# Performance work log

Measured on AMD Instinct MI355X. Metric: run time of the kernel, lower is better.

Reference implementation:

```python
import jax, jax.numpy as jnp
import numpy as np

N, E, D_X, D_H, K = 50000, 1600000, 128, 64, 4
NEG_SLOPE = 0.01  # torch nn.LeakyReLU() default


def setup_inputs() -> dict:
    key = jax.random.key(0)
    ks = jax.random.split(key, 8)
    x = jax.random.normal(ks[0], (N, D_X), dtype=jnp.float32)
    edge_index = jax.random.randint(ks[1], (2, E), 0, N, dtype=jnp.int64)
    s = 0.05
    Ww = jax.random.normal(ks[2], (K, D_H, D_X), dtype=jnp.float32) * s
    Wb = jax.random.normal(ks[3], (K, D_H), dtype=jnp.float32) * s
    aw = jax.random.normal(ks[4], (K, 1, 2 * D_H), dtype=jnp.float32) * s
    ab = jax.random.normal(ks[5], (K, 1), dtype=jnp.float32) * s
    Wo_w = jax.random.normal(ks[6], (D_H, K * D_H), dtype=jnp.float32) * s
    Wo_b = jax.random.normal(ks[7], (D_H,), dtype=jnp.float32) * s
    return {"edge_index": edge_index, "x": x, "Ww": Ww, "Wb": Wb,
            "aw": aw, "ab": ab, "Wo_w": Wo_w, "Wo_b": Wo_b}


def _single_head(x, src, dst, Ww_k, Wb_k, aw_k, ab_k):
    # Wx: [N, d_h] -- project once, gather per edge
    Wx = x @ Ww_k.T + Wb_k
    a_i = aw_k[0, :D_H]   # multiplies W(x_i) (target/dst)
    a_j = aw_k[0, D_H:]   # multiplies W(x_j) (source/src)
    si = Wx @ a_i         # [N]
    sj = Wx @ a_j         # [N]
    e = si[dst] + sj[src] + ab_k[0]                 # [E_tot]
    e = jnp.where(e >= 0, e, NEG_SLOPE * e)          # LeakyReLU
    # segment softmax over destination node (self-loops guarantee nonempty segments)
    m = jax.ops.segment_max(e, dst, num_segments=N)
    ex = jnp.exp(e - m[dst])
    den = jax.ops.segment_sum(ex, dst, num_segments=N)
    alpha = ex / den[dst]                            # [E_tot]
    msg = alpha[:, None] * Wx[src]                   # [E_tot, d_h]
    agg = jax.ops.segment_sum(msg, dst, num_segments=N)  # [N, d_h]
    # update(): softmax over the node dimension (dim=-2), as in the original
    return jax.nn.softmax(agg, axis=-2)


def reference(edge_index, x, Ww, Wb, aw, ab, Wo_w, Wo_b):
    n = x.shape[0]
    loops = jnp.tile(jnp.arange(n, dtype=edge_index.dtype)[None, :], (2, 1))
    ei = jnp.concatenate([edge_index, loops], axis=1)  # add_self_loops
    src, dst = ei[0], ei[1]  # x_j = x[src], x_i = x[dst]
    h_k = jax.vmap(lambda w, b, a, c: _single_head(x, src, dst, w, b, a, c))(Ww, Wb, aw, ab)  # [K, N, d_h]
    h_cat = jnp.transpose(h_k, (1, 0, 2)).reshape(n, K * D_H)
    return h_cat @ Wo_w.T + Wo_b
```

## Files before the change

kernel.cpp:

```cpp
#include <hip/hip_runtime.h>
#include <cfloat>

#define N_NODES 50000
#define N_EDGES 1600000
#define DX      128
#define DH      64
#define KH      4
#define NC      256
#define NEG_SLOPE 0.01f
#define SCAN_BLOCKS 196
#define BIN_BLOCKS 625
#define BIN_CHUNK  2560
#define BIN_CAP    10000

typedef float f2 __attribute__((ext_vector_type(2)));
typedef short s8v __attribute__((ext_vector_type(8)));
typedef float f4v __attribute__((ext_vector_type(4)));
typedef unsigned short ushort_t;

__device__ __forceinline__ unsigned pack_bf16(float a, float b) {
    unsigned ua = __float_as_uint(a), ub = __float_as_uint(b);
    ua = (ua + 0x7FFFu + ((ua >> 16) & 1u)) >> 16;
    ub = (ub + 0x7FFFu + ((ub >> 16) & 1u)) & 0xFFFF0000u;
    return ua | ub;
}
__device__ __forceinline__ float bflo(unsigned u) { return __uint_as_float(u << 16); }
__device__ __forceinline__ float bfhi(unsigned u) { return __uint_as_float(u & 0xFFFF0000u); }

__global__ void k_setup(const float* __restrict__ Ww, ushort_t* __restrict__ Bh,
                        ushort_t* __restrict__ Bl,
                        int* __restrict__ bcur, float* __restrict__ colsum) {
    int i = blockIdx.x * 256 + threadIdx.x;
    if (i < SCAN_BLOCKS) bcur[i] = i * BIN_CAP;
    if (i < NC) colsum[i] = 0.f;
    int e = i & 7, lane = (i >> 3) & 63, ct = (i >> 9) & 15, kt = (i >> 13) & 3;
    int k = kt * 32 + ((lane >> 4) << 3) + e;
    int c = ct * 16 + (lane & 15);
    float v = Ww[c * DX + k];
    unsigned uv = __float_as_uint(v);
    unsigned vh = (uv + 0x7FFFu + ((uv >> 16) & 1u)) >> 16;
    float rem = v - __uint_as_float(vh << 16);
    unsigned ur = __float_as_uint(rem);
    unsigned vl = (ur + 0x7FFFu + ((ur >> 16) & 1u)) >> 16;
    Bh[i] = (ushort_t)vh;
    Bl[i] = (ushort_t)vl;
}

__global__ void __launch_bounds__(256) k_gemm1(const float* __restrict__ x,
                                               const uint4* __restrict__ Bh,
                                               const uint4* __restrict__ Bl,
                                               const float* __restrict__ Wb,
                                               const float* __restrict__ aw,
                                               const float* __restrict__ ab,
                                               unsigned* __restrict__ Wx8,
                                               float* __restrict__ smeta,
                                               float* __restrict__ sic) {
    __shared__ float lds_wx[16][264];
    int n0b = blockIdx.x * 16;
    int wv = __builtin_amdgcn_readfirstlane(threadIdx.x >> 6);
    int lane = threadIdx.x & 63;
    int arow = lane & 15, agrp = lane >> 4;
    const float* xr = x + (size_t)(n0b + arow) * DX + agrp * 8;
    f4v acc[4];
#pragma unroll
    for (int ct = 0; ct < 4; ++ct) acc[ct] = {0.f, 0.f, 0.f, 0.f};

#pragma unroll
    for (int kt = 0; kt < 4; ++kt) {
        float4 xa = *(const float4*)(xr + kt * 32);
        float4 xb = *(const float4*)(xr + kt * 32 + 4);
        uint4 h, l;
        h.x = pack_bf16(xa.x, xa.y); h.y = pack_bf16(xa.z, xa.w);
        h.z = pack_bf16(xb.x, xb.y); h.w = pack_bf16(xb.z, xb.w);
        l.x = pack_bf16(xa.x - bflo(h.x), xa.y - bfhi(h.x));
        l.y = pack_bf16(xa.z - bflo(h.y), xa.w - bfhi(h.y));
        l.z = pack_bf16(xb.x - bflo(h.z), xb.y - bfhi(h.z));
        l.w = pack_bf16(xb.z - bflo(h.w), xb.w - bfhi(h.w));
        s8v ah = __builtin_bit_cast(s8v, h);
        s8v al = __builtin_bit_cast(s8v, l);
#pragma unroll
        for (int ct = 0; ct < 4; ++ct) {
            int ctg = wv * 4 + ct;
            uint4 bhv = Bh[(kt * 16 + ctg) * 64 + lane];
            uint4 blv = Bl[(kt * 16 + ctg) * 64 + lane];
            s8v bh8 = __builtin_bit_cast(s8v, bhv);
            s8v bl8 = __builtin_bit_cast(s8v, blv);
            acc[ct] = __builtin_amdgcn_mfma_f32_16x16x32_bf16(ah, bh8, acc[ct], 0, 0, 0);
            acc[ct] = __builtin_amdgcn_mfma_f32_16x16x32_bf16(al, bh8, acc[ct], 0, 0, 0);
            acc[ct] = __builtin_amdgcn_mfma_f32_16x16x32_bf16(ah, bl8, acc[ct], 0, 0, 0);
        }
    }
#pragma unroll
    for (int ct = 0; ct < 4; ++ct) {
        int c = wv * 64 + ct * 16 + arow;
        int r0 = agrp * 4;
        lds_wx[r0 + 0][c] = acc[ct].x;
        lds_wx[r0 + 1][c] = acc[ct].y;
        lds_wx[r0 + 2][c] = acc[ct].z;
        lds_wx[r0 + 3][c] = acc[ct].w;
    }
    __syncthreads();

    int kh = lane >> 4, lq = lane & 15;
    float4 bias = ((const float4*)Wb)[lane];
    const float* awi = aw + kh * 2 * DH + lq * 4;
    const float* awj = awi + DH;
    float ai0 = awi[0], ai1 = awi[1], ai2 = awi[2], ai3 = awi[3];
    float aj0 = awj[0], aj1 = awj[1], aj2 = awj[2], aj3 = awj[3];
    float abk = ab[kh];
#pragma unroll
    for (int rr = 0; rr < 4; ++rr) {
        int r = wv * 4 + rr;
        float4 o4 = *(float4*)&lds_wx[r][4 * lane];
        float o0 = o4.x + bias.x, o1 = o4.y + bias.y;
        float o2 = o4.z + bias.z, o3 = o4.w + bias.w;
        float pi = o0 * ai0 + o1 * ai1 + o2 * ai2 + o3 * ai3;
        float pj = o0 * aj0 + o1 * aj1 + o2 * aj2 + o3 * aj3;
        float am = fmaxf(fmaxf(fabsf(o0), fabsf(o1)), fmaxf(fabsf(o2), fabsf(o3)));
#pragma unroll
        for (int off = 8; off >= 1; off >>= 1) {
            pi += __shfl_xor(pi, off, 64);
            pj += __shfl_xor(pj, off, 64);
            am = fmaxf(am, __shfl_xor(am, off, 64));
        }
        am = fmaxf(am, 1e-20f);
        float rs = 127.f / am;
        int q0 = __float2int_rn(o0 * rs) + 128;
        int q1 = __float2int_rn(o1 * rs) + 128;
        int q2 = __float2int_rn(o2 * rs) + 128;
        int q3 = __float2int_rn(o3 * rs) + 128;
        unsigned pk = (unsigned)q0 | ((unsigned)q1 << 8) |
                      ((unsigned)q2 << 16) | ((unsigned)q3 << 24);
        Wx8[(size_t)(n0b + r) * 64 + lane] = pk;
        if (lq == 0) {
            sic[(n0b + r) * 4 + kh] = pi + abk;
            smeta[(size_t)(n0b + r) * 8 + kh] = pj;
            smeta[(size_t)(n0b + r) * 8 + 4 + kh] = am * (1.f / 127.f);
        }
    }
}

__global__ void __launch_bounds__(256) k_bin(const int* __restrict__ ei,
                                             int* __restrict__ bcur,
                                             unsigned* __restrict__ binned) {
    __shared__ int bh[SCAN_BLOCKS];
    __shared__ int bb[SCAN_BLOCKS];
    int t = threadIdx.x;
    if (t < SCAN_BLOCKS) bh[t] = 0;
    __syncthreads();
    int e0 = blockIdx.x * BIN_CHUNK;
#pragma unroll 5
    for (int k = 0; k < BIN_CHUNK / 256; ++k) {
        int dst = ei[N_EDGES + e0 + t + k * 256];
        atomicAdd(&bh[dst >> 8], 1);
    }
    __syncthreads();
    if (t < SCAN_BLOCKS) {
        bb[t] = atomicAdd(&bcur[t], bh[t]);
        bh[t] = 0;
    }
    __syncthreads();
#pragma unroll 5
    for (int k = 0; k < BIN_CHUNK / 256; ++k) {
        int e = e0 + t + k * 256;
        int src = ei[e];
        int dst = ei[N_EDGES + e];
        int b = dst >> 8;
        int lo = atomicAdd(&bh[b], 1);
        binned[bb[b] + lo] = (unsigned)src | ((unsigned)(dst & 255) << 16);
    }
}

__global__ void __launch_bounds__(1024) k_scatter3(const unsigned* __restrict__ binned,
                                                   const int* __restrict__ bcur,
                                                   int* __restrict__ rowstart,
                                                   int* __restrict__ rowend,
                                                   int* __restrict__ csr_src) {
    __shared__ int lcnt[256];
    __shared__ int lcur[256];
    __shared__ int s[256];
    int t = threadIdx.x, b = blockIdx.x;
    int e0 = b * BIN_CAP, e1 = bcur[b];
    if (t < 256) lcnt[t] = 0;
    __syncthreads();
    for (int i = e0 + t; i < e1; i += 1024)
        atomicAdd(&lcnt[binned[i] >> 16], 1);
    __syncthreads();
    int v = (t < 256) ? lcnt[t] : 0;
    if (t < 256) s[t] = v;
    __syncthreads();
#pragma unroll
    for (int off = 1; off < 256; off <<= 1) {
        int u = (t >= off && t < 256) ? s[t - off] : 0;
        __syncthreads();
        if (t < 256) s[t] += u;
        __syncthreads();
    }
    if (t < 256) {
        int d = b * 256 + t;
        int base_b = b * (BIN_CAP + 256);
        if (d < N_NODES) {
            int rs = base_b + (s[t] - v) + t;
            rowstart[d] = rs;
            rowend[d] = rs + 1 + v;
            csr_src[rs] = d;
            lcur[t] = rs + 1;
        } else lcur[t] = 0;
    }
    __syncthreads();
    for (int i = e0 + t; i < e1; i += 1024) {
        unsigned u = binned[i];
        int pos = atomicAdd(&lcur[u >> 16], 1);
        csr_src[pos] = (int)(u & 0xFFFFu);
    }
}

__global__ void __launch_bounds__(256) k_aggregate(const int* __restrict__ rowstart,
                                                   const int* __restrict__ rowend,
                                                   const int* __restrict__ csr_src,
                                                   const float* __restrict__ sic,
                                                   const float* __restrict__ smeta,
                                                   const unsigned* __restrict__ Wx8,
                                                   unsigned* __restrict__ expb) {
    __shared__ float exls[4][64 * 4];
    int wv = threadIdx.x >> 6;
    int dst = blockIdx.x * 4 + wv;
    int lane = threadIdx.x & 63;
    int kh = lane >> 4;
    int i0 = rowstart[dst], i1 = rowend[dst];
    float4 si = *(const float4*)&sic[(size_t)dst * 4];
    float* exl = exls[wv];
    const float* exb = exl + kh;
    const float4* sm4 = (const float4*)smeta;
    const char* wxp = (const char*)Wx8;
    size_t loff = (size_t)lane * 4;

    f2 acc01 = {0.f, 0.f}, acc23 = {0.f, 0.f};
    float den0 = 0.f, den1 = 0.f, den2 = 0.f, den3 = 0.f;
    float ds0 = 0.f, ds1 = 0.f, ds2 = 0.f, ds3 = 0.f;

    for (int b = i0; b < i1; b += 64) {
        int cnt = i1 - b;
        if (cnt > 64) cnt = 64;
        int ngrp = (cnt + 7) >> 3;
        int idx = b + lane;
        if (lane >= cnt) idx = i1 - 1;
        int sl = __builtin_nontemporal_load(&csr_src[idx]);
        float4 mj = sm4[(size_t)sl * 2];
        float4 ms = sm4[(size_t)sl * 2 + 1];
        unsigned gA[8], gB[8];
#pragma unroll
        for (int u = 0; u < 8; ++u) {
            int s = __builtin_amdgcn_readlane(sl, u);
            gA[u] = *(const unsigned*)(wxp + (((size_t)(unsigned)s) << 8) + loff);
        }
        if (ngrp > 1) {
#pragma unroll
            for (int u = 0; u < 8; ++u) {
                int s = __builtin_amdgcn_readlane(sl, 8 + u);
                gB[u] = *(const unsigned*)(wxp + (((size_t)(unsigned)s) << 8) + loff);
            }
        }
        float xs0 = 0.f, xs1 = 0.f, xs2 = 0.f, xs3 = 0.f;
        if (lane < cnt) {
            float e0 = si.x + mj.x, e1 = si.y + mj.y;
            float e2 = si.z + mj.z, e3 = si.w + mj.w;
            e0 = fmaxf(e0, NEG_SLOPE * e0);
            e1 = fmaxf(e1, NEG_SLOPE * e1);
            e2 = fmaxf(e2, NEG_SLOPE * e2);
            e3 = fmaxf(e3, NEG_SLOPE * e3);
            float ex0 = __expf(e0), ex1 = __expf(e1);
            float ex2 = __expf(e2), ex3 = __expf(e3);
            den0 += ex0; den1 += ex1; den2 += ex2; den3 += ex3;
            xs0 = ex0 * ms.x; xs1 = ex1 * ms.y;
            xs2 = ex2 * ms.z; xs3 = ex3 * ms.w;
            ds0 += xs0; ds1 += xs1; ds2 += xs2; ds3 += xs3;
        }
        *(float4*)&exl[lane * 4] = make_float4(xs0, xs1, xs2, xs3);
        asm volatile("" ::: "memory");
        for (int g = 0; g < ngrp; g += 2) {
#pragma unroll
            for (int u = 0; u < 8; ++u) {
                float ev = exb[(size_t)(g * 8 + u) * 4];
                f2 w01 = {(float)(gA[u] & 0xFFu), (float)((gA[u] >> 8) & 0xFFu)};
                f2 w23 = {(float)((gA[u] >> 16) & 0xFFu), (float)(gA[u] >> 24)};
                f2 e2 = {ev, ev};
                acc01 = __builtin_elementwise_fma(w01, e2, acc01);
                acc23 = __builtin_elementwise_fma(w23, e2, acc23);
            }
            if (g + 2 < ngrp) {
#pragma unroll
                for (int u = 0; u < 8; ++u) {
                    int s = __builtin_amdgcn_readlane(sl, (g + 2) * 8 + u);
                    gA[u] = *(const unsigned*)(wxp + (((size_t)(unsigned)s) << 8) + loff);
                }
            }
            if (g + 1 < ngrp) {
#pragma unroll
                for (int u = 0; u < 8; ++u) {
                    float ev = exb[(size_t)((g + 1) * 8 + u) * 4];
                    f2 w01 = {(float)(gB[u] & 0xFFu), (float)((gB[u] >> 8) & 0xFFu)};
                    f2 w23 = {(float)((gB[u] >> 16) & 0xFFu), (float)(gB[u] >> 24)};
                    f2 e2 = {ev, ev};
                    acc01 = __builtin_elementwise_fma(w01, e2, acc01);
                    acc23 = __builtin_elementwise_fma(w23, e2, acc23);
                }
                if (g + 3 < ngrp) {
#pragma unroll
                    for (int u = 0; u < 8; ++u) {
                        int s = __builtin_amdgcn_readlane(sl, (g + 3) * 8 + u);
                        gB[u] = *(const unsigned*)(wxp + (((size_t)(unsigned)s) << 8) + loff);
                    }
                }
            }
        }
        asm volatile("" ::: "memory");
    }

    den0 += __shfl_xor(den0, 16, 64); den0 += __shfl_xor(den0, 32, 64);
    den1 += __shfl_xor(den1, 16, 64); den1 += __shfl_xor(den1, 32, 64);
    den2 += __shfl_xor(den2, 16, 64); den2 += __shfl_xor(den2, 32, 64);
    den3 += __shfl_xor(den3, 16, 64); den3 += __shfl_xor(den3, 32, 64);
    ds0 += __shfl_xor(ds0, 16, 64); ds0 += __shfl_xor(ds0, 32, 64);
    ds1 += __shfl_xor(ds1, 16, 64); ds1 += __shfl_xor(ds1, 32, 64);
    ds2 += __shfl_xor(ds2, 16, 64); ds2 += __shfl_xor(ds2, 32, 64);
    ds3 += __shfl_xor(ds3, 16, 64); ds3 += __shfl_xor(ds3, 32, 64);
    float dsel  = (kh < 2) ? ((kh == 0) ? den0 : den1) : ((kh == 2) ? den2 : den3);
    float dssel = (kh < 2) ? ((kh == 0) ? ds0  : ds1)  : ((kh == 2) ? ds2  : ds3);
#pragma unroll
    for (int off = 1; off <= 8; off <<= 1) {
        dsel  += __shfl_xor(dsel, off, 64);
        dssel += __shfl_xor(dssel, off, 64);
    }

    float r = 1.f / dsel;
    float bias = 128.f * dssel;
    float o0 = __expf((acc01.x - bias) * r), o1 = __expf((acc01.y - bias) * r);
    float o2 = __expf((acc23.x - bias) * r), o3 = __expf((acc23.y - bias) * r);
    unsigned long long pk = (unsigned long long)pack_bf16(o0, o1) |
                            ((unsigned long long)pack_bf16(o2, o3) << 32);
    __builtin_nontemporal_store(pk,
        (unsigned long long*)&expb[(size_t)dst * 128 + lane * 2]);
}

__global__ void __launch_bounds__(256) k_colsum(const uint4* __restrict__ expb4,
                                                float* __restrict__ colsum) {
    __shared__ float part[8][256];
    int t = threadIdx.x;
    int q = t & 31, g = t >> 5;
    int r0 = blockIdx.x * 128;
    int r1 = min(r0 + 128, N_NODES);
    float s0 = 0.f, s1 = 0.f, s2 = 0.f, s3 = 0.f;
    float s4 = 0.f, s5 = 0.f, s6 = 0.f, s7 = 0.f;
    for (int r = r0 + g; r < r1; r += 8) {
        uint4 v = expb4[(size_t)r * 32 + q];
        s0 += bflo(v.x); s1 += bfhi(v.x);
        s2 += bflo(v.y); s3 += bfhi(v.y);
        s4 += bflo(v.z); s5 += bfhi(v.z);
        s6 += bflo(v.w); s7 += bfhi(v.w);
    }
    *(float4*)&part[g][8 * q]     = make_float4(s0, s1, s2, s3);
    *(float4*)&part[g][8 * q + 4] = make_float4(s4, s5, s6, s7);
    __syncthreads();
    float ps = part[0][t] + part[1][t] + part[2][t] + part[3][t]
             + part[4][t] + part[5][t] + part[6][t] + part[7][t];
    atomicAdd(&colsum[t], ps);
}

__global__ void k_prepWs(const float* __restrict__ Wo_w, const float* __restrict__ colsum,
                         ushort_t* __restrict__ Wsh, ushort_t* __restrict__ Wsl) {
    int i = blockIdx.x * 256 + threadIdx.x;
    int e = i & 7, lane = (i >> 3) & 63, ct = (i >> 9) & 3, kt = (i >> 11) & 7;
    int c = kt * 32 + ((lane >> 4) << 3) + e;
    int j = ct * 16 + (lane & 15);
    float v = Wo_w[j * NC + c] / colsum[c];
    unsigned uv = __float_as_uint(v);
    unsigned vh = (uv + 0x7FFFu + ((uv >> 16) & 1u)) >> 16;
    float rem = v - __uint_as_float(vh << 16);
    unsigned ur = __float_as_uint(rem);
    unsigned vl = (ur + 0x7FFFu + ((ur >> 16) & 1u)) >> 16;
    Wsh[i] = (ushort_t)vh;
    Wsl[i] = (ushort_t)vl;
}

__global__ void __launch_bounds__(256) k_out(const unsigned* __restrict__ expb,
                                             const uint4* __restrict__ Wsh,
                                             const uint4* __restrict__ Wsl,
                                             const float* __restrict__ Wo_b,
                                             float* __restrict__ out) {
    int n0 = blockIdx.x * 16;
    int wv = __builtin_amdgcn_readfirstlane(threadIdx.x >> 6);
    int lane = threadIdx.x & 63;
    int arow = lane & 15, agrp = lane >> 4;
    const unsigned* ar = expb + (size_t)(n0 + arow) * 128 + agrp * 4;
    f4v acc = {0.f, 0.f, 0.f, 0.f};
#pragma unroll
    for (int kt = 0; kt < 8; ++kt) {
        uint4 av = *(const uint4*)(ar + kt * 16);
        uint4 bh = Wsh[(kt * 4 + wv) * 64 + lane];
        uint4 bl = Wsl[(kt * 4 + wv) * 64 + lane];
        s8v a8 = __builtin_bit_cast(s8v, av);
        acc = __builtin_amdgcn_mfma_f32_16x16x32_bf16(a8, __builtin_bit_cast(s8v, bh), acc, 0, 0, 0);
        acc = __builtin_amdgcn_mfma_f32_16x16x32_bf16(a8, __builtin_bit_cast(s8v, bl), acc, 0, 0, 0);
    }
    int j = wv * 16 + arow;
    float bj = Wo_b[j];
#pragma unroll
    for (int r = 0; r < 4; ++r) {
        int node = n0 + agrp * 4 + r;
        out[(size_t)node * DH + j] = acc[r] + bj;
    }
}

extern "C" void kernel_launch(void* const* d_in, const int* in_sizes, int n_in,
                              void* d_out, int out_size, void* d_ws, size_t ws_size,
                              hipStream_t stream) {
    const int*   ei   = (const int*)d_in[0];
    const float* x    = (const float*)d_in[1];
    const float* Ww   = (const float*)d_in[2];
    const float* Wb   = (const float*)d_in[3];
    const float* aw   = (const float*)d_in[4];
    const float* ab   = (const float*)d_in[5];
    const float* Wo_w = (const float*)d_in[6];
    const float* Wo_b = (const float*)d_in[7];
    float* out = (float*)d_out;

    char* p = (char*)d_ws;
    auto alloc = [&](size_t bytes) -> char* {
        char* q = p;
        p += (bytes + 255) & ~(size_t)255;
        return q;
    };
    unsigned* Wx8      = (unsigned*)alloc((size_t)N_NODES * NC);
    unsigned* expb     = (unsigned*)alloc((size_t)N_NODES * NC * 2);
    ushort_t* Bh       = (ushort_t*)alloc((size_t)DX * NC * 2);
    ushort_t* Bl       = (ushort_t*)alloc((size_t)DX * NC * 2);
    ushort_t* Wsh      = (ushort_t*)alloc((size_t)NC * DH * 2);
    ushort_t* Wsl      = (ushort_t*)alloc((size_t)NC * DH * 2);
    float*    smeta    = (float*)alloc((size_t)N_NODES * 8 * 4);
    float*    sic      = (float*)alloc((size_t)N_NODES * 4 * 4);
    int*      rowstart = (int*)alloc((size_t)N_NODES * 4);
    int*      rowend   = (int*)alloc((size_t)N_NODES * 4);
    int*      csr_src  = (int*)alloc((size_t)SCAN_BLOCKS * (BIN_CAP + 256) * 4);
    unsigned* binned   = (unsigned*)alloc((size_t)SCAN_BLOCKS * BIN_CAP * 4);
    float*    colsum   = (float*)alloc(NC * 4);
    int*      bcur     = (int*)alloc(SCAN_BLOCKS * 4);

    k_setup<<<128, 256, 0, stream>>>(Ww, Bh, Bl, bcur, colsum);
    k_gemm1<<<N_NODES / 16, 256, 0, stream>>>(x, (const uint4*)Bh, (const uint4*)Bl,
                                              Wb, aw, ab, Wx8, smeta, sic);
    k_bin<<<BIN_BLOCKS, 256, 0, stream>>>(ei, bcur, binned);
    k_scatter3<<<SCAN_BLOCKS, 1024, 0, stream>>>(binned, bcur, rowstart, rowend, csr_src);
    k_aggregate<<<N_NODES / 4, 256, 0, stream>>>(rowstart, rowend, csr_src, sic, smeta,
                                                 Wx8, expb);
    k_colsum<<<(N_NODES + 127) / 128, 256, 0, stream>>>((const uint4*)expb, colsum);
    k_prepWs<<<(NC * DH) / 256, 256, 0, stream>>>(Wo_w, colsum, Wsh, Wsl);
    k_out<<<N_NODES / 16, 256, 0, stream>>>(expb, (const uint4*)Wsh, (const uint4*)Wsl,
                                            Wo_b, out);
}
```

Baseline: 262.0 us.

## Merge edge binning into GEMM launch and fold weight prep into colsum tail

```diff
diff --git a/kernel.cpp b/kernel.cpp
--- a/kernel.cpp
+++ b/kernel.cpp
@@ -12,6 +12,7 @@
 #define BIN_BLOCKS 625
 #define BIN_CHUNK  2560
 #define BIN_CAP    10000
+#define GEMM_BLOCKS (N_NODES / 16)
 
 typedef float f2 __attribute__((ext_vector_type(2)));
 typedef short s8v __attribute__((ext_vector_type(8)));
@@ -29,10 +30,12 @@
 
 __global__ void k_setup(const float* __restrict__ Ww, ushort_t* __restrict__ Bh,
                         ushort_t* __restrict__ Bl,
-                        int* __restrict__ bcur, float* __restrict__ colsum) {
+                        int* __restrict__ bcur, float* __restrict__ colsum,
+                        int* __restrict__ done) {
     int i = blockIdx.x * 256 + threadIdx.x;
     if (i < SCAN_BLOCKS) bcur[i] = i * BIN_CAP;
     if (i < NC) colsum[i] = 0.f;
+    if (i == 0) done[0] = 0;
     int e = i & 7, lane = (i >> 3) & 63, ct = (i >> 9) & 15, kt = (i >> 13) & 3;
     int k = kt * 32 + ((lane >> 4) << 3) + e;
     int c = ct * 16 + (lane & 15);
@@ -46,16 +49,50 @@
     Bl[i] = (ushort_t)vl;
 }
 
-__global__ void __launch_bounds__(256) k_gemm1(const float* __restrict__ x,
-                                               const uint4* __restrict__ Bh,
-                                               const uint4* __restrict__ Bl,
-                                               const float* __restrict__ Wb,
-                                               const float* __restrict__ aw,
-                                               const float* __restrict__ ab,
-                                               unsigned* __restrict__ Wx8,
-                                               float* __restrict__ smeta,
-                                               float* __restrict__ sic) {
+__global__ void __launch_bounds__(256) k_gemm1bin(const float* __restrict__ x,
+                                                  const uint4* __restrict__ Bh,
+                                                  const uint4* __restrict__ Bl,
+                                                  const float* __restrict__ Wb,
+                                                  const float* __restrict__ aw,
+                                                  const float* __restrict__ ab,
+                                                  unsigned* __restrict__ Wx8,
+                                                  float* __restrict__ smeta,
+                                                  float* __restrict__ sic,
+                                                  const int* __restrict__ ei,
+                                                  int* __restrict__ bcur,
+                                                  unsigned* __restrict__ binned) {
     __shared__ float lds_wx[16][264];
+    __shared__ int bh[SCAN_BLOCKS];
+    __shared__ int bb[SCAN_BLOCKS];
+
+    if (blockIdx.x >= GEMM_BLOCKS) {
+        int t = threadIdx.x;
+        if (t < SCAN_BLOCKS) bh[t] = 0;
+        __syncthreads();
+        int e0 = (blockIdx.x - GEMM_BLOCKS) * BIN_CHUNK;
+#pragma unroll 5
+        for (int k = 0; k < BIN_CHUNK / 256; ++k) {
+            int dst = ei[N_EDGES + e0 + t + k * 256];
+            atomicAdd(&bh[dst >> 8], 1);
+        }
+        __syncthreads();
+        if (t < SCAN_BLOCKS) {
+            bb[t] = atomicAdd(&bcur[t], bh[t]);
+            bh[t] = 0;
+        }
+        __syncthreads();
+#pragma unroll 5
+        for (int k = 0; k < BIN_CHUNK / 256; ++k) {
+            int e = e0 + t + k * 256;
+            int src = ei[e];
+            int dst = ei[N_EDGES + e];
+            int b = dst >> 8;
+            int lo = atomicAdd(&bh[b], 1);
+            binned[bb[b] + lo] = (unsigned)src | ((unsigned)(dst & 255) << 16);
+        }
+        return;
+    }
+
     int n0b = blockIdx.x * 16;
     int wv = __builtin_amdgcn_readfirstlane(threadIdx.x >> 6);
     int lane = threadIdx.x & 63;
@@ -137,37 +174,6 @@
             smeta[(size_t)(n0b + r) * 8 + kh] = pj;
             smeta[(size_t)(n0b + r) * 8 + 4 + kh] = am * (1.f / 127.f);
         }
-    }
-}
-
-__global__ void __launch_bounds__(256) k_bin(const int* __restrict__ ei,
-                                             int* __restrict__ bcur,
-                                             unsigned* __restrict__ binned) {
-    __shared__ int bh[SCAN_BLOCKS];
-    __shared__ int bb[SCAN_BLOCKS];
-    int t = threadIdx.x;
-    if (t < SCAN_BLOCKS) bh[t] = 0;
-    __syncthreads();
-    int e0 = blockIdx.x * BIN_CHUNK;
-#pragma unroll 5
-    for (int k = 0; k < BIN_CHUNK / 256; ++k) {
-        int dst = ei[N_EDGES + e0 + t + k * 256];
-        atomicAdd(&bh[dst >> 8], 1);
-    }
-    __syncthreads();
-    if (t < SCAN_BLOCKS) {
-        bb[t] = atomicAdd(&bcur[t], bh[t]);
-        bh[t] = 0;
-    }
-    __syncthreads();
-#pragma unroll 5
-    for (int k = 0; k < BIN_CHUNK / 256; ++k) {
-        int e = e0 + t + k * 256;
-        int src = ei[e];
-        int dst = ei[N_EDGES + e];
-        int b = dst >> 8;
-        int lo = atomicAdd(&bh[b], 1);
-        binned[bb[b] + lo] = (unsigned)src | ((unsigned)(dst & 255) << 16);
     }
 }
 
@@ -344,8 +350,13 @@
 }
 
 __global__ void __launch_bounds__(256) k_colsum(const uint4* __restrict__ expb4,
-                                                float* __restrict__ colsum) {
+                                                float* __restrict__ colsum,
+                                                const float* __restrict__ Wo_w,
+                                                ushort_t* __restrict__ Wsh,
+                                                ushort_t* __restrict__ Wsl,
+                                                int* __restrict__ done) {
     __shared__ float part[8][256];
+    __shared__ int lastflag;
     int t = threadIdx.x;
     int q = t & 31, g = t >> 5;
     int r0 = blockIdx.x * 128;
@@ -365,22 +376,26 @@
     float ps = part[0][t] + part[1][t] + part[2][t] + part[3][t]
              + part[4][t] + part[5][t] + part[6][t] + part[7][t];
     atomicAdd(&colsum[t], ps);
-}
-
-__global__ void k_prepWs(const float* __restrict__ Wo_w, const float* __restrict__ colsum,
-                         ushort_t* __restrict__ Wsh, ushort_t* __restrict__ Wsl) {
-    int i = blockIdx.x * 256 + threadIdx.x;
-    int e = i & 7, lane = (i >> 3) & 63, ct = (i >> 9) & 3, kt = (i >> 11) & 7;
-    int c = kt * 32 + ((lane >> 4) << 3) + e;
-    int j = ct * 16 + (lane & 15);
-    float v = Wo_w[j * NC + c] / colsum[c];
-    unsigned uv = __float_as_uint(v);
-    unsigned vh = (uv + 0x7FFFu + ((uv >> 16) & 1u)) >> 16;
-    float rem = v - __uint_as_float(vh << 16);
-    unsigned ur = __float_as_uint(rem);
-    unsigned vl = (ur + 0x7FFFu + ((ur >> 16) & 1u)) >> 16;
-    Wsh[i] = (ushort_t)vh;
-    Wsl[i] = (ushort_t)vl;
+
+    __threadfence();
+    if (t == 0) lastflag = (atomicAdd(done, 1) == (int)gridDim.x - 1);
+    __syncthreads();
+    if (lastflag) {
+        __threadfence();
+        for (int i = t; i < NC * DH; i += 256) {
+            int e = i & 7, lane = (i >> 3) & 63, ct = (i >> 9) & 3, kt = (i >> 11) & 7;
+            int c = kt * 32 + ((lane >> 4) << 3) + e;
+            int j = ct * 16 + (lane & 15);
+            float v = Wo_w[j * NC + c] / colsum[c];
+            unsigned uv = __float_as_uint(v);
+            unsigned vh = (uv + 0x7FFFu + ((uv >> 16) & 1u)) >> 16;
+            float rem = v - __uint_as_float(vh << 16);
+            unsigned ur = __float_as_uint(rem);
+            unsigned vl = (ur + 0x7FFFu + ((ur >> 16) & 1u)) >> 16;
+            Wsh[i] = (ushort_t)vh;
+            Wsl[i] = (ushort_t)vl;
+        }
+    }
 }
 
 __global__ void __launch_bounds__(256) k_out(const unsigned* __restrict__ expb,
@@ -445,16 +460,17 @@
     unsigned* binned   = (unsigned*)alloc((size_t)SCAN_BLOCKS * BIN_CAP * 4);
     float*    colsum   = (float*)alloc(NC * 4);
     int*      bcur     = (int*)alloc(SCAN_BLOCKS * 4);
-
-    k_setup<<<128, 256, 0, stream>>>(Ww, Bh, Bl, bcur, colsum);
-    k_gemm1<<<N_NODES / 16, 256, 0, stream>>>(x, (const uint4*)Bh, (const uint4*)Bl,
-                                              Wb, aw, ab, Wx8, smeta, sic);
-    k_bin<<<BIN_BLOCKS, 256, 0, stream>>>(ei, bcur, binned);
+    int*      done     = (int*)alloc(4);
+
+    k_setup<<<128, 256, 0, stream>>>(Ww, Bh, Bl, bcur, colsum, done);
+    k_gemm1bin<<<GEMM_BLOCKS + BIN_BLOCKS, 256, 0, stream>>>(
+        x, (const uint4*)Bh, (const uint4*)Bl, Wb, aw, ab, Wx8, smeta, sic,
+        ei, bcur, binned);
     k_scatter3<<<SCAN_BLOCKS, 1024, 0, stream>>>(binned, bcur, rowstart, rowend, csr_src);
     k_aggregate<<<N_NODES / 4, 256, 0, stream>>>(rowstart, rowend, csr_src, sic, smeta,
                                                  Wx8, expb);
-    k_colsum<<<(N_NODES + 127) / 128, 256, 0, stream>>>((const uint4*)expb, colsum);
-    k_prepWs<<<(NC * DH) / 256, 256, 0, stream>>>(Wo_w, colsum, Wsh, Wsl);
+    k_colsum<<<(N_NODES + 127) / 128, 256, 0, stream>>>((const uint4*)expb, colsum,
+                                                        Wo_w, Wsh, Wsl, done);
     k_out<<<N_NODES / 16, 256, 0, stream>>>(expb, (const uint4*)Wsh, (const uint4*)Wsl,
                                             Wo_b, out);
 }
```

Measured after the change: 296.2 us. 13.0% more time.

## Fuse node projection GEMM with edge binning and enlarge GEMM row tile

Applied to the files above, without the earlier changes.

```diff
diff --git a/kernel.cpp b/kernel.cpp
--- a/kernel.cpp
+++ b/kernel.cpp
@@ -12,6 +12,7 @@
 #define BIN_BLOCKS 625
 #define BIN_CHUNK  2560
 #define BIN_CAP    10000
+#define GEMM_BLOCKS 782
 
 typedef float f2 __attribute__((ext_vector_type(2)));
 typedef short s8v __attribute__((ext_vector_type(8)));
@@ -46,60 +47,93 @@
     Bl[i] = (ushort_t)vl;
 }
 
-__global__ void __launch_bounds__(256) k_gemm1(const float* __restrict__ x,
-                                               const uint4* __restrict__ Bh,
-                                               const uint4* __restrict__ Bl,
-                                               const float* __restrict__ Wb,
-                                               const float* __restrict__ aw,
-                                               const float* __restrict__ ab,
-                                               unsigned* __restrict__ Wx8,
-                                               float* __restrict__ smeta,
-                                               float* __restrict__ sic) {
+__global__ void __launch_bounds__(256) k_gemm1bin(const float* __restrict__ x,
+                                                  const uint4* __restrict__ Bh,
+                                                  const uint4* __restrict__ Bl,
+                                                  const float* __restrict__ Wb,
+                                                  const float* __restrict__ aw,
+                                                  const float* __restrict__ ab,
+                                                  unsigned* __restrict__ Wx8,
+                                                  float* __restrict__ smeta,
+                                                  float* __restrict__ sic,
+                                                  const int* __restrict__ ei,
+                                                  int* __restrict__ bcur,
+                                                  unsigned* __restrict__ binned) {
     __shared__ float lds_wx[16][264];
-    int n0b = blockIdx.x * 16;
+    __shared__ int bh[SCAN_BLOCKS];
+    __shared__ int bb[SCAN_BLOCKS];
+
+    if (blockIdx.x >= GEMM_BLOCKS) {
+        int t = threadIdx.x;
+        if (t < SCAN_BLOCKS) bh[t] = 0;
+        __syncthreads();
+        int e0 = (blockIdx.x - GEMM_BLOCKS) * BIN_CHUNK;
+#pragma unroll 5
+        for (int k = 0; k < BIN_CHUNK / 256; ++k) {
+            int dst = ei[N_EDGES + e0 + t + k * 256];
+            atomicAdd(&bh[dst >> 8], 1);
+        }
+        __syncthreads();
+        if (t < SCAN_BLOCKS) {
+            bb[t] = atomicAdd(&bcur[t], bh[t]);
+            bh[t] = 0;
+        }
+        __syncthreads();
+#pragma unroll 5
+        for (int k = 0; k < BIN_CHUNK / 256; ++k) {
+            int e = e0 + t + k * 256;
+            int src = ei[e];
+            int dst = ei[N_EDGES + e];
+            int b = dst >> 8;
+            int lo = atomicAdd(&bh[b], 1);
+            binned[bb[b] + lo] = (unsigned)src | ((unsigned)(dst & 255) << 16);
+        }
+        return;
+    }
+
+    int n0b = blockIdx.x * 64;
     int wv = __builtin_amdgcn_readfirstlane(threadIdx.x >> 6);
     int lane = threadIdx.x & 63;
     int arow = lane & 15, agrp = lane >> 4;
-    const float* xr = x + (size_t)(n0b + arow) * DX + agrp * 8;
-    f4v acc[4];
-#pragma unroll
-    for (int ct = 0; ct < 4; ++ct) acc[ct] = {0.f, 0.f, 0.f, 0.f};
+    f4v acc[4][4];
+#pragma unroll
+    for (int ct = 0; ct < 4; ++ct)
+#pragma unroll
+        for (int ng = 0; ng < 4; ++ng) acc[ct][ng] = {0.f, 0.f, 0.f, 0.f};
 
 #pragma unroll
     for (int kt = 0; kt < 4; ++kt) {
-        float4 xa = *(const float4*)(xr + kt * 32);
-        float4 xb = *(const float4*)(xr + kt * 32 + 4);
-        uint4 h, l;
-        h.x = pack_bf16(xa.x, xa.y); h.y = pack_bf16(xa.z, xa.w);
-        h.z = pack_bf16(xb.x, xb.y); h.w = pack_bf16(xb.z, xb.w);
-        l.x = pack_bf16(xa.x - bflo(h.x), xa.y - bfhi(h.x));
-        l.y = pack_bf16(xa.z - bflo(h.y), xa.w - bfhi(h.y));
-        l.z = pack_bf16(xb.x - bflo(h.z), xb.y - bfhi(h.z));
-        l.w = pack_bf16(xb.z - bflo(h.w), xb.w - bfhi(h.w));
-        s8v ah = __builtin_bit_cast(s8v, h);
-        s8v al = __builtin_bit_cast(s8v, l);
+        s8v bh8[4], bl8[4];
 #pragma unroll
         for (int ct = 0; ct < 4; ++ct) {
             int ctg = wv * 4 + ct;
-            uint4 bhv = Bh[(kt * 16 + ctg) * 64 + lane];
-            uint4 blv = Bl[(kt * 16 + ctg) * 64 + lane];
-            s8v bh8 = __builtin_bit_cast(s8v, bhv);
-            s8v bl8 = __builtin_bit_cast(s8v, blv);
-            acc[ct] = __builtin_amdgcn_mfma_f32_16x16x32_bf16(ah, bh8, acc[ct], 0, 0, 0);
-            acc[ct] = __builtin_amdgcn_mfma_f32_16x16x32_bf16(al, bh8, acc[ct], 0, 0, 0);
-            acc[ct] = __builtin_amdgcn_mfma_f32_16x16x32_bf16(ah, bl8, acc[ct], 0, 0, 0);
-        }
-    }
-#pragma unroll
-    for (int ct = 0; ct < 4; ++ct) {
-        int c = wv * 64 + ct * 16 + arow;
-        int r0 = agrp * 4;
-        lds_wx[r0 + 0][c] = acc[ct].x;
-        lds_wx[r0 + 1][c] = acc[ct].y;
-        lds_wx[r0 + 2][c] = acc[ct].z;
-        lds_wx[r0 + 3][c] = acc[ct].w;
-    }
-    __syncthreads();
+            bh8[ct] = __builtin_bit_cast(s8v, Bh[(kt * 16 + ctg) * 64 + lane]);
+            bl8[ct] = __builtin_bit_cast(s8v, Bl[(kt * 16 + ctg) * 64 + lane]);
+        }
+#pragma unroll
+        for (int ng = 0; ng < 4; ++ng) {
+            int node = n0b + ng * 16 + arow;
+            if (node > N_NODES - 1) node = N_NODES - 1;
+            const float* xr = x + (size_t)node * DX + agrp * 8 + kt * 32;
+            float4 xa = *(const float4*)xr;
+            float4 xb = *(const float4*)(xr + 4);
+            uint4 h, l;
+            h.x = pack_bf16(xa.x, xa.y); h.y = pack_bf16(xa.z, xa.w);
+            h.z = pack_bf16(xb.x, xb.y); h.w = pack_bf16(xb.z, xb.w);
+            l.x = pack_bf16(xa.x - bflo(h.x), xa.y - bfhi(h.x));
+            l.y = pack_bf16(xa.z - bflo(h.y), xa.w - bfhi(h.y));
+            l.z = pack_bf16(xb.x - bflo(h.z), xb.y - bfhi(h.z));
+            l.w = pack_bf16(xb.z - bflo(h.w), xb.w - bfhi(h.w));
+            s8v ah = __builtin_bit_cast(s8v, h);
+            s8v al = __builtin_bit_cast(s8v, l);
+#pragma unroll
+            for (int ct = 0; ct < 4; ++ct) {
+                acc[ct][ng] = __builtin_amdgcn_mfma_f32_16x16x32_bf16(ah, bh8[ct], acc[ct][ng], 0, 0, 0);
+                acc[ct][ng] = __builtin_amdgcn_mfma_f32_16x16x32_bf16(al, bh8[ct], acc[ct][ng], 0, 0, 0);
+                acc[ct][ng] = __builtin_amdgcn_mfma_f32_16x16x32_bf16(ah, bl8[ct], acc[ct][ng], 0, 0, 0);
+            }
+        }
+    }
 
     int kh = lane >> 4, lq = lane & 15;
     float4 bias = ((const float4*)Wb)[lane];
@@ -109,65 +143,51 @@
     float aj0 = awj[0], aj1 = awj[1], aj2 = awj[2], aj3 = awj[3];
     float abk = ab[kh];
 #pragma unroll
-    for (int rr = 0; rr < 4; ++rr) {
-        int r = wv * 4 + rr;
-        float4 o4 = *(float4*)&lds_wx[r][4 * lane];
-        float o0 = o4.x + bias.x, o1 = o4.y + bias.y;
-        float o2 = o4.z + bias.z, o3 = o4.w + bias.w;
-        float pi = o0 * ai0 + o1 * ai1 + o2 * ai2 + o3 * ai3;
-        float pj = o0 * aj0 + o1 * aj1 + o2 * aj2 + o3 * aj3;
-        float am = fmaxf(fmaxf(fabsf(o0), fabsf(o1)), fmaxf(fabsf(o2), fabsf(o3)));
-#pragma unroll
-        for (int off = 8; off >= 1; off >>= 1) {
-            pi += __shfl_xor(pi, off, 64);
-            pj += __shfl_xor(pj, off, 64);
-            am = fmaxf(am, __shfl_xor(am, off, 64));
-        }
-        am = fmaxf(am, 1e-20f);
-        float rs = 127.f / am;
-        int q0 = __float2int_rn(o0 * rs) + 128;
-        int q1 = __float2int_rn(o1 * rs) + 128;
-        int q2 = __float2int_rn(o2 * rs) + 128;
-        int q3 = __float2int_rn(o3 * rs) + 128;
-        unsigned pk = (unsigned)q0 | ((unsigned)q1 << 8) |
-                      ((unsigned)q2 << 16) | ((unsigned)q3 << 24);
-        Wx8[(size_t)(n0b + r) * 64 + lane] = pk;
-        if (lq == 0) {
-            sic[(n0b + r) * 4 + kh] = pi + abk;
-            smeta[(size_t)(n0b + r) * 8 + kh] = pj;
-            smeta[(size_t)(n0b + r) * 8 + 4 + kh] = am * (1.f / 127.f);
-        }
-    }
-}
-
-__global__ void __launch_bounds__(256) k_bin(const int* __restrict__ ei,
-                                             int* __restrict__ bcur,
-                                             unsigned* __restrict__ binned) {
-    __shared__ int bh[SCAN_BLOCKS];
-    __shared__ int bb[SCAN_BLOCKS];
-    int t = threadIdx.x;
-    if (t < SCAN_BLOCKS) bh[t] = 0;
-    __syncthreads();
-    int e0 = blockIdx.x * BIN_CHUNK;
-#pragma unroll 5
-    for (int k = 0; k < BIN_CHUNK / 256; ++k) {
-        int dst = ei[N_EDGES + e0 + t + k * 256];
-        atomicAdd(&bh[dst >> 8], 1);
-    }
-    __syncthreads();
-    if (t < SCAN_BLOCKS) {
-        bb[t] = atomicAdd(&bcur[t], bh[t]);
-        bh[t] = 0;
-    }
-    __syncthreads();
-#pragma unroll 5
-    for (int k = 0; k < BIN_CHUNK / 256; ++k) {
-        int e = e0 + t + k * 256;
-        int src = ei[e];
-        int dst = ei[N_EDGES + e];
-        int b = dst >> 8;
-        int lo = atomicAdd(&bh[b], 1);
-        binned[bb[b] + lo] = (unsigned)src | ((unsigned)(dst & 255) << 16);
+    for (int ng = 0; ng < 4; ++ng) {
+        __syncthreads();
+#pragma unroll
+        for (int ct = 0; ct < 4; ++ct) {
+            int c = wv * 64 + ct * 16 + arow;
+            int r0 = agrp * 4;
+            lds_wx[r0 + 0][c] = acc[ct][ng].x;
+            lds_wx[r0 + 1][c] = acc[ct][ng].y;
+            lds_wx[r0 + 2][c] = acc[ct][ng].z;
+            lds_wx[r0 + 3][c] = acc[ct][ng].w;
+        }
+        __syncthreads();
+#pragma unroll
+        for (int rr = 0; rr < 4; ++rr) {
+            int r = wv * 4 + rr;
+            int node = n0b + ng * 16 + r;
+            float4 o4 = *(float4*)&lds_wx[r][4 * lane];
+            float o0 = o4.x + bias.x, o1 = o4.y + bias.y;
+            float o2 = o4.z + bias.z, o3 = o4.w + bias.w;
+            float pi = o0 * ai0 + o1 * ai1 + o2 * ai2 + o3 * ai3;
+            float pj = o0 * aj0 + o1 * aj1 + o2 * aj2 + o3 * aj3;
+            float am = fmaxf(fmaxf(fabsf(o0), fabsf(o1)), fmaxf(fabsf(o2), fabsf(o3)));
+#pragma unroll
+            for (int off = 8; off >= 1; off >>= 1) {
+                pi += __shfl_xor(pi, off, 64);
+                pj += __shfl_xor(pj, off, 64);
+                am = fmaxf(am, __shfl_xor(am, off, 64));
+            }
+            am = fmaxf(am, 1e-20f);
+            float rs = 127.f / am;
+            int q0 = __float2int_rn(o0 * rs) + 128;
+            int q1 = __float2int_rn(o1 * rs) + 128;
+            int q2 = __float2int_rn(o2 * rs) + 128;
+            int q3 = __float2int_rn(o3 * rs) + 128;
+            unsigned pk = (unsigned)q0 | ((unsigned)q1 << 8) |
+                          ((unsigned)q2 << 16) | ((unsigned)q3 << 24);
+            if (node < N_NODES) {
+                Wx8[(size_t)node * 64 + lane] = pk;
+                if (lq == 0) {
+                    sic[(size_t)node * 4 + kh] = pi + abk;
+                    smeta[(size_t)node * 8 + kh] = pj;
+                    smeta[(size_t)node * 8 + 4 + kh] = am * (1.f / 127.f);
+                }
+            }
+        }
     }
 }
 
@@ -447,9 +467,9 @@
     int*      bcur     = (int*)alloc(SCAN_BLOCKS * 4);
 
     k_setup<<<128, 256, 0, stream>>>(Ww, Bh, Bl, bcur, colsum);
-    k_gemm1<<<N_NODES / 16, 256, 0, stream>>>(x, (const uint4*)Bh, (const uint4*)Bl,
-                                              Wb, aw, ab, Wx8, smeta, sic);
-    k_bin<<<BIN_BLOCKS, 256, 0, stream>>>(ei, bcur, binned);
+    k_gemm1bin<<<GEMM_BLOCKS + BIN_BLOCKS, 256, 0, stream>>>(
+        x, (const uint4*)Bh, (const uint4*)Bl, Wb, aw, ab, Wx8, smeta, sic,
+        ei, bcur, binned);
     k_scatter3<<<SCAN_BLOCKS, 1024, 0, stream>>>(binned, bcur, rowstart, rowend, csr_src);
     k_aggregate<<<N_NODES / 4, 256, 0, stream>>>(rowstart, rowend, csr_src, sic, smeta,
                                                  Wx8, expb);
```

New measurement: 246.9 us. 5.8% less time.
